# Kernel tuning notes

Hardware: AMD Instinct MI355X
Metric: run time of the kernel (lower is better)

## Reference

```python
import jax, jax.numpy as jnp
import numpy as np

B, S, DIN, D, H, DOUT, W = 4, 2048, 256, 512, 8, 128, 64
HD = D // H


def setup_inputs() -> dict:
    key = jax.random.key(0)
    ks = jax.random.split(key, 16)
    r = lambda k, shape, s=0.02: (jax.random.normal(k, shape, jnp.float32) * s)
    return dict(
        x=jax.random.normal(ks[0], (B, S, DIN), jnp.float32),
        pos=jax.random.normal(ks[1], (1, S, D), jnp.float32),  # torch.randn init
        win_w=r(ks[2], (DIN, D)), win_b=jnp.zeros((D,), jnp.float32),
        l_wqkv=r(ks[3], (3, D, D)), l_bqkv=jnp.zeros((3, D), jnp.float32),
        l_wo=r(ks[4], (D, D)), l_bo=jnp.zeros((D,), jnp.float32),
        g_wqkv=r(ks[5], (3, D, D)), g_bqkv=jnp.zeros((3, D), jnp.float32),
        g_wo=r(ks[6], (D, D)), g_bo=jnp.zeros((D,), jnp.float32),
        gate_w=r(ks[7], (2 * D, D)), gate_b=jnp.zeros((D,), jnp.float32),
        ffn_w1=r(ks[8], (D, 2 * D)), ffn_b1=jnp.zeros((2 * D,), jnp.float32),
        ffn_w2=r(ks[9], (2 * D, D)), ffn_b2=jnp.zeros((D,), jnp.float32),
        n1_g=jnp.ones((D,), jnp.float32), n1_b=jnp.zeros((D,), jnp.float32),
        n2_g=jnp.ones((D,), jnp.float32), n2_b=jnp.zeros((D,), jnp.float32),
        n3_g=jnp.ones((D,), jnp.float32), n3_b=jnp.zeros((D,), jnp.float32),
        out_w=r(ks[10], (D, DOUT)), out_b=jnp.zeros((DOUT,), jnp.float32),
    )


def _ln(x, g, b, eps=1e-5):
    m = x.mean(-1, keepdims=True)
    v = ((x - m) ** 2).mean(-1, keepdims=True)
    return (x - m) * jax.lax.rsqrt(v + eps) * g + b


def _mha(x, wqkv, bqkv, wo, bo, mask):
    b, s, d = x.shape
    q = (x @ wqkv[0] + bqkv[0]).reshape(b, s, H, HD)
    k = (x @ wqkv[1] + bqkv[1]).reshape(b, s, H, HD)
    v = (x @ wqkv[2] + bqkv[2]).reshape(b, s, H, HD)
    scores = jnp.einsum('bqhd,bkhd->bhqk', q, k) / np.sqrt(HD).astype(np.float32)
    if mask is not None:
        scores = scores + mask  # additive -inf band mask
    attn = jax.nn.softmax(scores, axis=-1)
    o = jnp.einsum('bhqk,bkhd->bqhd', attn, v).reshape(b, s, d)
    return o @ wo + bo


def reference(x, pos, win_w, win_b,
              l_wqkv, l_bqkv, l_wo, l_bo,
              g_wqkv, g_bqkv, g_wo, g_bo,
              gate_w, gate_b, ffn_w1, ffn_b1, ffn_w2, ffn_b2,
              n1_g, n1_b, n2_g, n2_b, n3_g, n3_b, out_w, out_b):
    s = x.shape[1]
    # band mask: row i allows cols [i - W//2, i + W//2] (matches create_local_mask)
    idx = jnp.arange(s)
    band = jnp.abs(idx[:, None] - idx[None, :]) <= (W // 2)
    mask = jnp.where(band, 0.0, -jnp.inf).astype(jnp.float32)

    h = x @ win_w + win_b + pos
    local_out = _mha(h, l_wqkv, l_bqkv, l_wo, l_bo, mask)
    global_out = _mha(h, g_wqkv, g_bqkv, g_wo, g_bo, None)

    combined = jnp.concatenate([local_out, global_out], axis=-1)
    gate = jnp.tanh(jax.nn.relu(combined @ gate_w + gate_b))
    fused = gate * local_out + (1.0 - gate) * global_out

    h = _ln(h + fused, n1_g, n1_b)
    ffn = jax.nn.relu(h @ ffn_w1 + ffn_b1) @ ffn_w2 + ffn_b2
    h = _ln(h + ffn, n2_g, n2_b)
    h = _ln(h, n3_g, n3_b)
    pooled = h.mean(axis=1)  # AdaptiveAvgPool1d(1) over seq
    return pooled @ out_w + out_b
```

## Files before the change

### kernel.cpp

```cpp
#include <hip/hip_runtime.h>
#include <math.h>
#include <stdint.h>

#define S_LEN 2048
#define DMODEL 512
#define NHEAD 8
#define BATCH 4
#define M_ROWS (BATCH * S_LEN)
#define UAC 4194304

typedef __attribute__((ext_vector_type(8))) short frag8;
typedef __attribute__((ext_vector_type(4))) float f32x4;

__device__ inline unsigned short f2bf(float f) {
    unsigned int u = __float_as_uint(f);
    return (unsigned short)((u + 0x7FFFu + ((u >> 16) & 1u)) >> 16);
}
__device__ inline float bf2f(unsigned short h) {
    return __uint_as_float(((unsigned int)h) << 16);
}

#if __has_builtin(__builtin_amdgcn_exp2f)
#define EXP2(x) __builtin_amdgcn_exp2f(x)
#else
#define EXP2(x) __expf(0.6931471805599453f * (x))
#endif

#if __has_builtin(__builtin_amdgcn_global_load_lds)
__device__ __forceinline__ void glds16(const void* g, void* l, int lane) {
    __builtin_amdgcn_global_load_lds(
        (__attribute__((address_space(1))) void*)(uintptr_t)g,
        (__attribute__((address_space(3))) void*)(uintptr_t)l, 16, 0, 0);
    (void)lane;
}
#else
__device__ __forceinline__ void glds16(const void* g, void* l, int lane) {
    ((uint4*)l)[lane] = ((const uint4*)g)[0];
}
#endif

struct WSeg { const float* src; unsigned short* dst; int K; int N; int start; };
struct WTab { WSeg s[12]; };

__global__ __launch_bounds__(256) void wcast_all(WTab tab)
{
    __shared__ float t[32][33];
    const int bid = blockIdx.x;
    int si = 0;
#pragma unroll
    for (int i = 1; i < 12; ++i) if (bid >= tab.s[i].start) si = i;
    const WSeg sg = tab.s[si];
    const int tile = bid - sg.start;
    const int nk = sg.K >> 5;
    const int k0 = (tile % nk) * 32, n0 = (tile / nk) * 32;
    {
        int kk = threadIdx.x >> 3, nq = (threadIdx.x & 7) * 4;
        float4 v = *(const float4*)&sg.src[(size_t)(k0 + kk) * sg.N + n0 + nq];
        t[kk][nq + 0] = v.x; t[kk][nq + 1] = v.y; t[kk][nq + 2] = v.z; t[kk][nq + 3] = v.w;
    }
    __syncthreads();
    {
        int n = threadIdx.x >> 3, kq = (threadIdx.x & 7) * 4;
        ushort4 o;
        o.x = f2bf(t[kq + 0][n]); o.y = f2bf(t[kq + 1][n]);
        o.z = f2bf(t[kq + 2][n]); o.w = f2bf(t[kq + 3][n]);
        *(ushort4*)&sg.dst[(size_t)(n0 + n) * sg.K + k0 + kq] = o;
    }
}

__global__ __launch_bounds__(256) void castx_kernel(
    const float* __restrict__ x, unsigned short* __restrict__ xb)
{
    const size_t i = ((size_t)blockIdx.x * 256 + threadIdx.x) * 8;
    float4 a = *(const float4*)&x[i], b = *(const float4*)&x[i + 4];
    unsigned short us[8];
    us[0] = f2bf(a.x); us[1] = f2bf(a.y); us[2] = f2bf(a.z); us[3] = f2bf(a.w);
    us[4] = f2bf(b.x); us[5] = f2bf(b.y); us[6] = f2bf(b.z); us[7] = f2bf(b.w);
    *(uint4*)&xb[i] = *(uint4*)us;
}

__global__ __launch_bounds__(256) void vtrans2_kernel(
    const unsigned short* __restrict__ Vl, const unsigned short* __restrict__ Vg,
    unsigned short* __restrict__ VTl, unsigned short* __restrict__ VTg)
{
    __shared__ unsigned short T[64][72];
    const unsigned short* V = blockIdx.z ? Vg : Vl;
    unsigned short* Vt = blockIdx.z ? VTg : VTl;
    const int st = blockIdx.x, bh = blockIdx.y;
    const int b = bh >> 3, h = bh & 7;
    const int tid = threadIdx.x;
    {
        const int s = tid >> 2, d0 = (tid & 3) * 16;
        const unsigned short* src = V + ((size_t)(b * S_LEN + st * 64 + s) * DMODEL + h * 64 + d0);
        *(uint4*)&T[s][d0] = *(const uint4*)src;
        *(uint4*)&T[s][d0 + 8] = *(const uint4*)(src + 8);
    }
    __syncthreads();
    {
        const int d = tid >> 2, s0 = (tid & 3) * 16;
        unsigned short buf[16];
#pragma unroll
        for (int j = 0; j < 16; ++j) buf[j] = T[s0 + j][d];
        unsigned short* dst = Vt + ((size_t)(bh * 64 + d) * S_LEN + st * 64 + s0);
        *(uint4*)&dst[0] = *(const uint4*)&buf[0];
        *(uint4*)&dst[8] = *(const uint4*)&buf[8];
    }
}

template <int MODE, int BN>
__global__ __launch_bounds__(256) void gemm_mfma(
    const unsigned short* __restrict__ A, const unsigned short* __restrict__ A2,
    const unsigned short* __restrict__ Wt, const float* __restrict__ bias,
    const float* __restrict__ bias2, const float* __restrict__ pos,
    unsigned short* __restrict__ C, unsigned short* __restrict__ C2,
    int M, int N, int K)
{
    constexpr int UN = BN / 32;
    __shared__ unsigned short As[128 * 64];
    __shared__ unsigned short Bs[BN * 64];
    const int tid = threadIdx.x;
    const int wave = tid >> 6, lane = tid & 63;
    const int lr = lane & 15, quad = lane >> 4;
    const int bm = blockIdx.x * 128, bn = blockIdx.y * BN;
    const int rm = (wave >> 1) * 64, rn = (wave & 1) * (BN / 2);
    const int Khalf = K >> 1;
    const int KA = (MODE == 3) ? Khalf : K;

    const unsigned short* SA = A;
    const unsigned short* SW = Wt;
    const float* SBIAS = bias;
    unsigned short* SC = C;
    if constexpr (MODE == 6) {
        if (blockIdx.z) { SA = A2; SW = Wt + 512 * 512; SBIAS = bias2; SC = C2; }
    }

    const int lrow = lane >> 3;
    const int gch = ((lane & 7) - lrow) & 7;
    const size_t laneA = (size_t)(bm + wave * 32 + lrow) * KA + gch * 8;
    const size_t laneB = (size_t)(bn + wave * (BN / 4) + lrow) * K + gch * 8;
    unsigned short* ldsA = As + wave * 2048;
    unsigned short* ldsB = Bs + wave * (BN * 16);

    f32x4 acc[4][UN];
#pragma unroll
    for (int t = 0; t < 4; ++t)
#pragma unroll
        for (int u = 0; u < UN; ++u) acc[t][u] = (f32x4){0.f, 0.f, 0.f, 0.f};

    const int sw0 = ((quad + lr) & 7) * 8;
    const int sw1 = ((quad + lr + 4) & 7) * 8;

    for (int k0 = 0; k0 < K; k0 += 64) {
        __syncthreads();
        const unsigned short* Ab; int kadj;
        if constexpr (MODE == 3) { Ab = (k0 < Khalf) ? A : A2; kadj = k0 & (Khalf - 1); }
        else { Ab = SA; kadj = k0; }
        const unsigned short* pa = Ab + laneA + kadj;
        glds16(pa,           ldsA,        lane);
        glds16(pa + 8 * KA,  ldsA + 512,  lane);
        glds16(pa + 16 * KA, ldsA + 1024, lane);
        glds16(pa + 24 * KA, ldsA + 1536, lane);
        const unsigned short* pb = SW + laneB + k0;
#pragma unroll
        for (int i = 0; i < UN; ++i)
            glds16(pb + i * 8 * K, ldsB + i * 512, lane);
        __syncthreads();

#pragma unroll
        for (int kc = 0; kc < 2; ++kc) {
            const int sw = kc ? sw1 : sw0;
            frag8 af[4], bf[UN];
#pragma unroll
            for (int t = 0; t < 4; ++t)
                af[t] = *(const frag8*)&As[(rm + t * 16 + lr) * 64 + sw];
#pragma unroll
            for (int u = 0; u < UN; ++u)
                bf[u] = *(const frag8*)&Bs[(rn + u * 16 + lr) * 64 + sw];
#pragma unroll
            for (int t = 0; t < 4; ++t)
#pragma unroll
                for (int u = 0; u < UN; ++u)
                    acc[t][u] = __builtin_amdgcn_mfma_f32_16x16x32_bf16(
                        af[t], bf[u], acc[t][u], 0, 0, 0);
        }
    }

#pragma unroll
    for (int t = 0; t < 4; ++t) {
#pragma unroll
        for (int i = 0; i < 4; ++i) {
            const int m = bm + rm + t * 16 + quad * 4 + i;
#pragma unroll
            for (int u = 0; u < UN; ++u) {
                const int n = bn + rn + u * 16 + lr;
                if constexpr (MODE == 5) {
                    const int mat = n >> 9;
                    const int nn = n & 511;
                    const float* bp = (mat < 3) ? (bias + (mat << 9))
                                                : (bias2 + ((mat - 3) << 9));
                    float v = acc[t][u][i] + bp[nn];
                    if (mat == 0 || mat == 3) v *= 0.18033688011112042f;
                    C[(size_t)mat * UAC + (size_t)m * DMODEL + nn] = f2bf(v);
                } else {
                    float v = acc[t][u][i] + SBIAS[n];
                    if constexpr (MODE == 1) v += pos[(size_t)(m & (S_LEN - 1)) * N + n];
                    if constexpr (MODE == 2) v = fmaxf(v, 0.0f);
                    if constexpr (MODE == 3) {
                        float g = tanhf(fmaxf(v, 0.0f));
                        float lo = bf2f(A[(size_t)m * Khalf + n]);
                        float go = bf2f(A2[(size_t)m * Khalf + n]);
                        v = g * lo + (1.0f - g) * go;
                    }
                    SC[(size_t)m * N + n] = f2bf(v);
                }
            }
        }
    }
}

__global__ __launch_bounds__(256) void attn_mfma(
    const unsigned short* __restrict__ Ql, const unsigned short* __restrict__ Kl,
    const unsigned short* __restrict__ VTl, unsigned short* __restrict__ Ol,
    const unsigned short* __restrict__ Qg, const unsigned short* __restrict__ Kg,
    const unsigned short* __restrict__ VTg, unsigned short* __restrict__ Og)
{
    __shared__ unsigned short Ks[64 * 64];
    __shared__ unsigned short Vts[64 * 64];
    __shared__ unsigned short Ps[128 * 64];
    const int qt = blockIdx.x, h = blockIdx.y;
    const int glob = blockIdx.z >> 2, b = blockIdx.z & 3;
    const int masked = !glob;
    const unsigned short* Q  = glob ? Qg  : Ql;
    const unsigned short* Kv = glob ? Kg  : Kl;
    const unsigned short* Vt = glob ? VTg : VTl;
    unsigned short* O        = glob ? Og  : Ol;
    const int tid = threadIdx.x;
    const int wave = tid >> 6, lane = tid & 63;
    const int lr = lane & 15, quad = lane >> 4;

    {
        const int q = tid >> 1, cb = (tid & 1) * 4;
        const unsigned short* src = Q + ((size_t)(b * S_LEN + qt * 128 + q) * DMODEL + h * 64 + cb * 8);
#pragma unroll
        for (int i = 0; i < 4; ++i)
            *(uint4*)&Ps[q * 64 + (((cb + i + q) & 7) * 8)] = *(const uint4*)(src + i * 8);
    }
    const int sw0 = ((quad + lr) & 7) * 8;
    const int sw1 = ((quad + lr + 4) & 7) * 8;
    const int ws32 = wave * 32;
    frag8 qf[2][2];
#pragma unroll
    for (int s = 0; s < 2; ++s) {
        qf[s][0] = *(const frag8*)&Ps[(ws32 + s * 16 + lr) * 64 + sw0];
        qf[s][1] = *(const frag8*)&Ps[(ws32 + s * 16 + lr) * 64 + sw1];
    }

    f32x4 oacc[2][4];
#pragma unroll
    for (int s = 0; s < 2; ++s)
#pragma unroll
        for (int t = 0; t < 4; ++t) oacc[s][t] = (f32x4){0.f, 0.f, 0.f, 0.f};
    float l_r[2] = {0.f, 0.f};

    int kt0 = 0, kt1 = 31;
    if (masked) {
        kt0 = qt * 128 >= 32 ? (qt * 128 - 32) >> 6 : 0;
        int hi = (qt * 128 + 127 + 32) >> 6;
        kt1 = hi < 31 ? hi : 31;
    }

    const int lrow = lane >> 3;
    const int gch = ((lane & 7) - lrow) & 7;
    const unsigned short* kp = Kv + ((size_t)(b * S_LEN + kt0 * 64 + wave * 16 + lrow) * DMODEL + h * 64 + gch * 8);
    const unsigned short* vp = Vt + ((size_t)((b * 8 + h) * 64 + wave * 16 + lrow) * S_LEN + kt0 * 64 + gch * 8);
    unsigned short* lk = Ks + wave * 1024;
    unsigned short* lv = Vts + wave * 1024;

    for (int kt = kt0; kt <= kt1; ++kt) {
        __syncthreads();
        glds16(kp, lk, lane);
        glds16(kp + 8 * DMODEL, lk + 512, lane);
        glds16(vp, lv, lane);
        glds16(vp + 8 * S_LEN, lv + 512, lane);
        kp += 64 * DMODEL; vp += 64;
        __syncthreads();

        f32x4 sacc[2][4];
#pragma unroll
        for (int s = 0; s < 2; ++s)
#pragma unroll
            for (int t = 0; t < 4; ++t) sacc[s][t] = (f32x4){0.f, 0.f, 0.f, 0.f};
#pragma unroll
        for (int kc = 0; kc < 2; ++kc) {
            const int sw = kc ? sw1 : sw0;
#pragma unroll
            for (int t = 0; t < 4; ++t) {
                frag8 kf = *(const frag8*)&Ks[(t * 16 + lr) * 64 + sw];
                sacc[0][t] = __builtin_amdgcn_mfma_f32_16x16x32_bf16(kf, qf[0][kc], sacc[0][t], 0, 0, 0);
                sacc[1][t] = __builtin_amdgcn_mfma_f32_16x16x32_bf16(kf, qf[1][kc], sacc[1][t], 0, 0, 0);
            }
        }

#pragma unroll
        for (int s = 0; s < 2; ++s) {
            const int prow = (ws32 + s * 16 + lr) * 64;
#pragma unroll
            for (int t = 0; t < 4; ++t) {
                float p0 = EXP2(sacc[s][t][0]);
                float p1 = EXP2(sacc[s][t][1]);
                float p2 = EXP2(sacc[s][t][2]);
                float p3 = EXP2(sacc[s][t][3]);
                if (masked) {
                    const int qa = qt * 128 + ws32 + s * 16 + lr;
                    const int ca = kt * 64 + t * 16 + quad * 4;
                    int d0 = qa - ca;
                    if (d0 > 32 || d0 < -32) p0 = 0.f;
                    int d1 = qa - (ca + 1);
                    if (d1 > 32 || d1 < -32) p1 = 0.f;
                    int d2 = qa - (ca + 2);
                    if (d2 > 32 || d2 < -32) p2 = 0.f;
                    int d3 = qa - (ca + 3);
                    if (d3 > 32 || d3 < -32) p3 = 0.f;
                }
                const unsigned u0 = __float_as_uint(p0) & 0xFFFF0000u;
                const unsigned u1 = __float_as_uint(p1) & 0xFFFF0000u;
                const unsigned u2 = __float_as_uint(p2) & 0xFFFF0000u;
                const unsigned u3 = __float_as_uint(p3) & 0xFFFF0000u;
                l_r[s] += (__uint_as_float(u0) + __uint_as_float(u1)) +
                          (__uint_as_float(u2) + __uint_as_float(u3));
                uint2 pw;
                pw.x = __builtin_amdgcn_perm(u1, u0, 0x07060302);
                pw.y = __builtin_amdgcn_perm(u3, u2, 0x07060302);
                const int slot = ((2 * t + (quad >> 1) + lr) & 7) * 8 + (quad & 1) * 4;
                *(uint2*)&Ps[prow + slot] = pw;
            }
        }

#pragma unroll
        for (int cc = 0; cc < 2; ++cc) {
            const int sw = cc ? sw1 : sw0;
            frag8 pa0 = *(const frag8*)&Ps[(ws32 + lr) * 64 + sw];
            frag8 pa1 = *(const frag8*)&Ps[(ws32 + 16 + lr) * 64 + sw];
#pragma unroll
            for (int t = 0; t < 4; ++t) {
                frag8 vf = *(const frag8*)&Vts[(t * 16 + lr) * 64 + sw];
                oacc[0][t] = __builtin_amdgcn_mfma_f32_16x16x32_bf16(pa0, vf, oacc[0][t], 0, 0, 0);
                oacc[1][t] = __builtin_amdgcn_mfma_f32_16x16x32_bf16(pa1, vf, oacc[1][t], 0, 0, 0);
            }
        }
    }

#pragma unroll
    for (int s = 0; s < 2; ++s) {
        float l = l_r[s];
        l += __shfl_xor(l, 16);
        l += __shfl_xor(l, 32);
#pragma unroll
        for (int i = 0; i < 4; ++i) {
            const float inv = 1.0f / __shfl(l, quad * 4 + i);
            const int q = qt * 128 + ws32 + s * 16 + quad * 4 + i;
#pragma unroll
            for (int t = 0; t < 4; ++t)
                O[(size_t)(b * S_LEN + q) * DMODEL + h * 64 + t * 16 + lr] =
                    f2bf(oacc[s][t][i] * inv);
        }
    }
}

__device__ inline float wave_sum64(float v) {
#pragma unroll
    for (int off = 1; off < 64; off <<= 1) v += __shfl_xor(v, off);
    return v;
}

__global__ __launch_bounds__(256) void ln_res_kernel(
    const unsigned short* __restrict__ A, const unsigned short* __restrict__ Bb,
    const float* __restrict__ g, const float* __restrict__ be,
    unsigned short* __restrict__ out)
{
    const size_t row = blockIdx.x * 4 + (threadIdx.x >> 6);
    const int lane = threadIdx.x & 63;
    float x[8]; float s = 0.f;
#pragma unroll
    for (int k = 0; k < 8; ++k) {
        size_t idx = row * DMODEL + k * 64 + lane;
        x[k] = bf2f(A[idx]) + bf2f(Bb[idx]);
        s += x[k];
    }
    s = wave_sum64(s);
    float mean = s * (1.0f / DMODEL);
    float v = 0.f;
#pragma unroll
    for (int k = 0; k < 8; ++k) { float d = x[k] - mean; v += d * d; }
    v = wave_sum64(v) * (1.0f / DMODEL);
    float r = rsqrtf(v + 1e-5f);
#pragma unroll
    for (int k = 0; k < 8; ++k)
        out[row * DMODEL + k * 64 + lane] =
            f2bf((x[k] - mean) * r * g[k * 64 + lane] + be[k * 64 + lane]);
}

__global__ __launch_bounds__(256) void ln_double_kernel(
    const unsigned short* __restrict__ A, const unsigned short* __restrict__ Bb,
    const float* __restrict__ g2, const float* __restrict__ b2,
    const float* __restrict__ g3, const float* __restrict__ b3,
    unsigned short* __restrict__ out)
{
    const size_t row = blockIdx.x * 4 + (threadIdx.x >> 6);
    const int lane = threadIdx.x & 63;
    float x[8]; float s = 0.f;
#pragma unroll
    for (int k = 0; k < 8; ++k) {
        size_t idx = row * DMODEL + k * 64 + lane;
        x[k] = bf2f(A[idx]) + bf2f(Bb[idx]);
        s += x[k];
    }
    s = wave_sum64(s);
    float mean = s * (1.0f / DMODEL);
    float v = 0.f;
#pragma unroll
    for (int k = 0; k < 8; ++k) { float d = x[k] - mean; v += d * d; }
    v = wave_sum64(v) * (1.0f / DMODEL);
    float r = rsqrtf(v + 1e-5f);
    float t[8]; float s2 = 0.f;
#pragma unroll
    for (int k = 0; k < 8; ++k) {
        t[k] = (x[k] - mean) * r * g2[k * 64 + lane] + b2[k * 64 + lane];
        s2 += t[k];
    }
    s2 = wave_sum64(s2);
    float mean2 = s2 * (1.0f / DMODEL);
    float v2 = 0.f;
#pragma unroll
    for (int k = 0; k < 8; ++k) { float d = t[k] - mean2; v2 += d * d; }
    v2 = wave_sum64(v2) * (1.0f / DMODEL);
    float r2 = rsqrtf(v2 + 1e-5f);
#pragma unroll
    for (int k = 0; k < 8; ++k)
        out[row * DMODEL + k * 64 + lane] =
            f2bf((t[k] - mean2) * r2 * g3[k * 64 + lane] + b3[k * 64 + lane]);
}

__global__ __launch_bounds__(256) void pool_kernel(
    const unsigned short* __restrict__ h2, float* __restrict__ pooled)
{
    const int b = blockIdx.x >> 4;
    const int chunk = blockIdx.x & 15;
    const int tid = threadIdx.x;
    float s0 = 0.f, s1 = 0.f;
    size_t base = (size_t)(b * S_LEN + chunk * 128) * DMODEL;
    for (int r = 0; r < 128; ++r) {
        s0 += bf2f(h2[base + (size_t)r * DMODEL + tid]);
        s1 += bf2f(h2[base + (size_t)r * DMODEL + 256 + tid]);
    }
    atomicAdd(&pooled[b * DMODEL + tid], s0);
    atomicAdd(&pooled[b * DMODEL + 256 + tid], s1);
}

__global__ __launch_bounds__(128) void out_kernel(
    const float* __restrict__ pooled, const float* __restrict__ w,
    const float* __restrict__ bias, float* __restrict__ out)
{
    const int b = blockIdx.x;
    const int o = threadIdx.x;
    float acc = 0.f;
    for (int d = 0; d < DMODEL; ++d)
        acc += pooled[b * DMODEL + d] * w[d * 128 + o];
    out[b * 128 + o] = acc * (1.0f / S_LEN) + bias[o];
}

extern "C" void kernel_launch(void* const* d_in, const int* in_sizes, int n_in,
                              void* d_out, int out_size, void* d_ws, size_t ws_size,
                              hipStream_t stream)
{
    const float* x      = (const float*)d_in[0];
    const float* pos    = (const float*)d_in[1];
    const float* win_w  = (const float*)d_in[2];
    const float* win_b  = (const float*)d_in[3];
    const float* l_wqkv = (const float*)d_in[4];
    const float* l_bqkv = (const float*)d_in[5];
    const float* l_wo   = (const float*)d_in[6];
    const float* l_bo   = (const float*)d_in[7];
    const float* g_wqkv = (const float*)d_in[8];
    const float* g_bqkv = (const float*)d_in[9];
    const float* g_wo   = (const float*)d_in[10];
    const float* g_bo   = (const float*)d_in[11];
    const float* gate_w = (const float*)d_in[12];
    const float* gate_b = (const float*)d_in[13];
    const float* ffn_w1 = (const float*)d_in[14];
    const float* ffn_b1 = (const float*)d_in[15];
    const float* ffn_w2 = (const float*)d_in[16];
    const float* ffn_b2 = (const float*)d_in[17];
    const float* n1_g   = (const float*)d_in[18];
    const float* n1_b   = (const float*)d_in[19];
    const float* n2_g   = (const float*)d_in[20];
    const float* n2_b   = (const float*)d_in[21];
    const float* n3_g   = (const float*)d_in[22];
    const float* n3_b   = (const float*)d_in[23];
    const float* out_w  = (const float*)d_in[24];
    const float* out_b  = (const float*)d_in[25];
    float* out = (float*)d_out;

    unsigned short* ws16 = (unsigned short*)d_ws;
    const size_t UA = (size_t)UAC;
    unsigned short* H    = ws16 + 0 * UA;
    unsigned short* QKV  = ws16 + 1 * UA;
    unsigned short* Ql   = ws16 + 1 * UA;
    unsigned short* Kl   = ws16 + 2 * UA;
    unsigned short* Vl   = ws16 + 3 * UA;
    unsigned short* Qg   = ws16 + 4 * UA;
    unsigned short* Kg   = ws16 + 5 * UA;
    unsigned short* Vg   = ws16 + 6 * UA;
    unsigned short* VTl  = ws16 + 7 * UA;
    unsigned short* AOl    = Vl;
    unsigned short* LO     = Kl;
    unsigned short* GO     = Qg;
    unsigned short* FUSED  = Kg;
    unsigned short* H1     = Vg;
    unsigned short* FFNMID = Vl;
    unsigned short* FFNOUT = Ql;
    unsigned short* H2     = Kl;
    float* POOLED = (float*)(void*)H;

    unsigned short* wt = ws16 + 8 * UA;
    unsigned short* win_t  = wt;
    unsigned short* lqkv_t = win_t  + 131072;
    unsigned short* gqkv_t = lqkv_t + 786432;
    unsigned short* lwo_t  = gqkv_t + 786432;
    unsigned short* gwo_t  = lwo_t  + 262144;
    unsigned short* gate_t = gwo_t  + 262144;
    unsigned short* ffn1_t = gate_t + 524288;
    unsigned short* ffn2_t = ffn1_t + 524288;
    unsigned short* xb     = ffn2_t + 524288;
    unsigned short* VTg    = xb + 2097152;
    unsigned short* AOg    = VTg + UA;

    WTab tab;
    tab.s[0]  = {win_w,             win_t,             256,  512,    0};
    tab.s[1]  = {l_wqkv + 0*262144, lqkv_t + 0*262144, 512,  512,  128};
    tab.s[2]  = {l_wqkv + 1*262144, lqkv_t + 1*262144, 512,  512,  384};
    tab.s[3]  = {l_wqkv + 2*262144, lqkv_t + 2*262144, 512,  512,  640};
    tab.s[4]  = {g_wqkv + 0*262144, gqkv_t + 0*262144, 512,  512,  896};
    tab.s[5]  = {g_wqkv + 1*262144, gqkv_t + 1*262144, 512,  512, 1152};
    tab.s[6]  = {g_wqkv + 2*262144, gqkv_t + 2*262144, 512,  512, 1408};
    tab.s[7]  = {l_wo,              lwo_t,             512,  512, 1664};
    tab.s[8]  = {g_wo,              gwo_t,             512,  512, 1920};
    tab.s[9]  = {gate_w,            gate_t,            1024, 512, 2176};
    tab.s[10] = {ffn_w1,            ffn1_t,            512, 1024, 2688};
    tab.s[11] = {ffn_w2,            ffn2_t,            1024, 512, 3200};

    dim3 blk(256);
    castx_kernel<<<dim3(1024), blk, 0, stream>>>(x, xb);
    wcast_all<<<dim3(3712), blk, 0, stream>>>(tab);

    dim3 gD(M_ROWS / 128, 512 / 64);
    dim3 gW(M_ROWS / 128, 512 / 64, 2);
    dim3 gQ(M_ROWS / 128, 3072 / 128);
    dim3 gF(M_ROWS / 128, 1024 / 128);
    dim3 gAT(S_LEN / 128, NHEAD, 2*BATCH);
    dim3 gV(S_LEN / 64, BATCH * NHEAD, 2);

    gemm_mfma<1, 64><<<gD, blk, 0, stream>>>(xb, nullptr, win_t, win_b, nullptr, pos, H, nullptr, M_ROWS, 512, 256);

    gemm_mfma<5, 128><<<gQ, blk, 0, stream>>>(H, nullptr, lqkv_t, l_bqkv, g_bqkv, nullptr, QKV, nullptr, M_ROWS, 3072, 512);

    vtrans2_kernel<<<gV, blk, 0, stream>>>(Vl, Vg, VTl, VTg);

    attn_mfma<<<gAT, blk, 0, stream>>>(Ql, Kl, VTl, AOl, Qg, Kg, VTg, AOg);

    gemm_mfma<6, 64><<<gW, blk, 0, stream>>>(AOl, AOg, lwo_t, l_bo, g_bo, nullptr, LO, GO, M_ROWS, 512, 512);

    gemm_mfma<3, 64><<<gD, blk, 0, stream>>>(LO, GO, gate_t, gate_b, nullptr, nullptr, FUSED, nullptr, M_ROWS, 512, 1024);

    ln_res_kernel<<<M_ROWS / 4, blk, 0, stream>>>(H, FUSED, n1_g, n1_b, H1);

    gemm_mfma<2, 128><<<gF, blk, 0, stream>>>(H1, nullptr, ffn1_t, ffn_b1, nullptr, nullptr, FFNMID, nullptr, M_ROWS, 1024, 512);
    gemm_mfma<0, 64><<<gD, blk, 0, stream>>>(FFNMID, nullptr, ffn2_t, ffn_b2, nullptr, nullptr, FFNOUT, nullptr, M_ROWS, 512, 1024);

    ln_double_kernel<<<M_ROWS / 4, blk, 0, stream>>>(H1, FFNOUT, n2_g, n2_b, n3_g, n3_b, H2);

    hipMemsetAsync(POOLED, 0, BATCH * DMODEL * sizeof(float), stream);
    pool_kernel<<<dim3(BATCH * 16), blk, 0, stream>>>(H2, POOLED);
    out_kernel<<<dim3(BATCH), dim3(128), 0, stream>>>(POOLED, out_w, out_b, out);
}
```

Baseline: 368.6 us.

## Split attention into local and global kernels with double-buffered KV

Replaces the combined local/global attention kernel with two specialized kernels. The local kernel uses 64-row query tiles so each block visits only three KV tiles, which cuts wasted band work and removes the masked/unmasked branching. The global kernel drops the mask code and double-buffers K/V tiles in LDS so the next tile's loads overlap the current tile's compute. The trade-offs are an extra kernel launch, the two attention types no longer sharing one grid, and doubled LDS use in the global kernel, which may lower occupancy.

```diff
diff --git a/kernel.cpp b/kernel.cpp
--- a/kernel.cpp
+++ b/kernel.cpp
@@ -218,56 +218,38 @@
     }
 }
 
-__global__ __launch_bounds__(256) void attn_mfma(
-    const unsigned short* __restrict__ Ql, const unsigned short* __restrict__ Kl,
-    const unsigned short* __restrict__ VTl, unsigned short* __restrict__ Ol,
-    const unsigned short* __restrict__ Qg, const unsigned short* __restrict__ Kg,
-    const unsigned short* __restrict__ VTg, unsigned short* __restrict__ Og)
+__global__ __launch_bounds__(256) void attn_local(
+    const unsigned short* __restrict__ Q, const unsigned short* __restrict__ Kv,
+    const unsigned short* __restrict__ Vt, unsigned short* __restrict__ O)
 {
     __shared__ unsigned short Ks[64 * 64];
     __shared__ unsigned short Vts[64 * 64];
-    __shared__ unsigned short Ps[128 * 64];
-    const int qt = blockIdx.x, h = blockIdx.y;
-    const int glob = blockIdx.z >> 2, b = blockIdx.z & 3;
-    const int masked = !glob;
-    const unsigned short* Q  = glob ? Qg  : Ql;
-    const unsigned short* Kv = glob ? Kg  : Kl;
-    const unsigned short* Vt = glob ? VTg : VTl;
-    unsigned short* O        = glob ? Og  : Ol;
+    __shared__ unsigned short Ps[64 * 64];
+    const int qt = blockIdx.x, h = blockIdx.y, b = blockIdx.z;
     const int tid = threadIdx.x;
     const int wave = tid >> 6, lane = tid & 63;
     const int lr = lane & 15, quad = lane >> 4;
 
     {
-        const int q = tid >> 1, cb = (tid & 1) * 4;
-        const unsigned short* src = Q + ((size_t)(b * S_LEN + qt * 128 + q) * DMODEL + h * 64 + cb * 8);
-#pragma unroll
-        for (int i = 0; i < 4; ++i)
-            *(uint4*)&Ps[q * 64 + (((cb + i + q) & 7) * 8)] = *(const uint4*)(src + i * 8);
+        const int q = tid >> 2, c8 = (tid & 3) * 2;
+        const unsigned short* src = Q + ((size_t)(b * S_LEN + qt * 64 + q) * DMODEL + h * 64 + c8 * 8);
+        *(uint4*)&Ps[q * 64 + (((c8 + q) & 7) * 8)] = *(const uint4*)src;
+        *(uint4*)&Ps[q * 64 + (((c8 + 1 + q) & 7) * 8)] = *(const uint4*)(src + 8);
     }
     const int sw0 = ((quad + lr) & 7) * 8;
     const int sw1 = ((quad + lr + 4) & 7) * 8;
-    const int ws32 = wave * 32;
-    frag8 qf[2][2];
-#pragma unroll
-    for (int s = 0; s < 2; ++s) {
-        qf[s][0] = *(const frag8*)&Ps[(ws32 + s * 16 + lr) * 64 + sw0];
-        qf[s][1] = *(const frag8*)&Ps[(ws32 + s * 16 + lr) * 64 + sw1];
-    }
-
-    f32x4 oacc[2][4];
-#pragma unroll
-    for (int s = 0; s < 2; ++s)
-#pragma unroll
-        for (int t = 0; t < 4; ++t) oacc[s][t] = (f32x4){0.f, 0.f, 0.f, 0.f};
-    float l_r[2] = {0.f, 0.f};
-
-    int kt0 = 0, kt1 = 31;
-    if (masked) {
-        kt0 = qt * 128 >= 32 ? (qt * 128 - 32) >> 6 : 0;
-        int hi = (qt * 128 + 127 + 32) >> 6;
-        kt1 = hi < 31 ? hi : 31;
-    }
+    const int prow = (wave * 16 + lr) * 64;
+    frag8 qf[2];
+    qf[0] = *(const frag8*)&Ps[prow + sw0];
+    qf[1] = *(const frag8*)&Ps[prow + sw1];
+
+    f32x4 oacc[4];
+#pragma unroll
+    for (int t = 0; t < 4; ++t) oacc[t] = (f32x4){0.f, 0.f, 0.f, 0.f};
+    float l_r = 0.f;
+
+    const int kt0 = qt > 0 ? qt - 1 : 0;
+    const int kt1 = qt < 31 ? qt + 1 : 31;
 
     const int lrow = lane >> 3;
     const int gch = ((lane & 7) - lrow) & 7;
@@ -285,17 +267,142 @@
         kp += 64 * DMODEL; vp += 64;
         __syncthreads();
 
-        f32x4 sacc[2][4];
-#pragma unroll
-        for (int s = 0; s < 2; ++s)
-#pragma unroll
-            for (int t = 0; t < 4; ++t) sacc[s][t] = (f32x4){0.f, 0.f, 0.f, 0.f};
+        f32x4 sacc[4];
+#pragma unroll
+        for (int t = 0; t < 4; ++t) sacc[t] = (f32x4){0.f, 0.f, 0.f, 0.f};
 #pragma unroll
         for (int kc = 0; kc < 2; ++kc) {
             const int sw = kc ? sw1 : sw0;
 #pragma unroll
             for (int t = 0; t < 4; ++t) {
                 frag8 kf = *(const frag8*)&Ks[(t * 16 + lr) * 64 + sw];
+                sacc[t] = __builtin_amdgcn_mfma_f32_16x16x32_bf16(kf, qf[kc], sacc[t], 0, 0, 0);
+            }
+        }
+
+#pragma unroll
+        for (int t = 0; t < 4; ++t) {
+            float p0 = EXP2(sacc[t][0]);
+            float p1 = EXP2(sacc[t][1]);
+            float p2 = EXP2(sacc[t][2]);
+            float p3 = EXP2(sacc[t][3]);
+            const int qa = qt * 64 + wave * 16 + lr;
+            const int ca = kt * 64 + t * 16 + quad * 4;
+            int d0 = qa - ca;
+            if (d0 > 32 || d0 < -32) p0 = 0.f;
+            int d1 = qa - (ca + 1);
+            if (d1 > 32 || d1 < -32) p1 = 0.f;
+            int d2 = qa - (ca + 2);
+            if (d2 > 32 || d2 < -32) p2 = 0.f;
+            int d3 = qa - (ca + 3);
+            if (d3 > 32 || d3 < -32) p3 = 0.f;
+            const unsigned u0 = __float_as_uint(p0) & 0xFFFF0000u;
+            const unsigned u1 = __float_as_uint(p1) & 0xFFFF0000u;
+            const unsigned u2 = __float_as_uint(p2) & 0xFFFF0000u;
+            const unsigned u3 = __float_as_uint(p3) & 0xFFFF0000u;
+            l_r += (__uint_as_float(u0) + __uint_as_float(u1)) +
+                   (__uint_as_float(u2) + __uint_as_float(u3));
+            uint2 pw;
+            pw.x = __builtin_amdgcn_perm(u1, u0, 0x07060302);
+            pw.y = __builtin_amdgcn_perm(u3, u2, 0x07060302);
+            const int slot = ((2 * t + (quad >> 1) + lr) & 7) * 8 + (quad & 1) * 4;
+            *(uint2*)&Ps[prow + slot] = pw;
+        }
+
+#pragma unroll
+        for (int cc = 0; cc < 2; ++cc) {
+            const int sw = cc ? sw1 : sw0;
+            frag8 pa = *(const frag8*)&Ps[prow + sw];
+#pragma unroll
+            for (int t = 0; t < 4; ++t) {
+                frag8 vf = *(const frag8*)&Vts[(t * 16 + lr) * 64 + sw];
+                oacc[t] = __builtin_amdgcn_mfma_f32_16x16x32_bf16(pa, vf, oacc[t], 0, 0, 0);
+            }
+        }
+    }
+
+    l_r += __shfl_xor(l_r, 16);
+    l_r += __shfl_xor(l_r, 32);
+#pragma unroll
+    for (int i = 0; i < 4; ++i) {
+        const float inv = 1.0f / __shfl(l_r, quad * 4 + i);
+        const int q = qt * 64 + wave * 16 + quad * 4 + i;
+#pragma unroll
+        for (int t = 0; t < 4; ++t)
+            O[(size_t)(b * S_LEN + q) * DMODEL + h * 64 + t * 16 + lr] = f2bf(oacc[t][i] * inv);
+    }
+}
+
+#define ISSUE_KV_G(KT, BUF) do {                                                \
+    const unsigned short* _kp = kbase + (size_t)(KT) * (64 * DMODEL);           \
+    const unsigned short* _vp = vbase + (size_t)(KT) * 64;                      \
+    unsigned short* _lk = Ks + (BUF) * 4096 + wave * 1024;                      \
+    unsigned short* _lv = Vts + (BUF) * 4096 + wave * 1024;                     \
+    glds16(_kp, _lk, lane); glds16(_kp + 8 * DMODEL, _lk + 512, lane);          \
+    glds16(_vp, _lv, lane); glds16(_vp + 8 * S_LEN, _lv + 512, lane);           \
+} while (0)
+
+__global__ __launch_bounds__(256) void attn_global(
+    const unsigned short* __restrict__ Q, const unsigned short* __restrict__ Kv,
+    const unsigned short* __restrict__ Vt, unsigned short* __restrict__ O)
+{
+    __shared__ unsigned short Ks[2 * 64 * 64];
+    __shared__ unsigned short Vts[2 * 64 * 64];
+    __shared__ unsigned short Ps[128 * 64];
+    const int qt = blockIdx.x, h = blockIdx.y, b = blockIdx.z;
+    const int tid = threadIdx.x;
+    const int wave = tid >> 6, lane = tid & 63;
+    const int lr = lane & 15, quad = lane >> 4;
+
+    {
+        const int q = tid >> 1, cb = (tid & 1) * 4;
+        const unsigned short* src = Q + ((size_t)(b * S_LEN + qt * 128 + q) * DMODEL + h * 64 + cb * 8);
+#pragma unroll
+        for (int i = 0; i < 4; ++i)
+            *(uint4*)&Ps[q * 64 + (((cb + i + q) & 7) * 8)] = *(const uint4*)(src + i * 8);
+    }
+    const int sw0 = ((quad + lr) & 7) * 8;
+    const int sw1 = ((quad + lr + 4) & 7) * 8;
+    const int ws32 = wave * 32;
+    frag8 qf[2][2];
+#pragma unroll
+    for (int s = 0; s < 2; ++s) {
+        qf[s][0] = *(const frag8*)&Ps[(ws32 + s * 16 + lr) * 64 + sw0];
+        qf[s][1] = *(const frag8*)&Ps[(ws32 + s * 16 + lr) * 64 + sw1];
+    }
+
+    f32x4 oacc[2][4];
+#pragma unroll
+    for (int s = 0; s < 2; ++s)
+#pragma unroll
+        for (int t = 0; t < 4; ++t) oacc[s][t] = (f32x4){0.f, 0.f, 0.f, 0.f};
+    float l_r[2] = {0.f, 0.f};
+
+    const int lrow = lane >> 3;
+    const int gch = ((lane & 7) - lrow) & 7;
+    const unsigned short* kbase = Kv + ((size_t)(b * S_LEN + wave * 16 + lrow) * DMODEL + h * 64 + gch * 8);
+    const unsigned short* vbase = Vt + ((size_t)((b * 8 + h) * 64 + wave * 16 + lrow) * S_LEN + gch * 8);
+
+    ISSUE_KV_G(0, 0);
+
+    for (int it = 0; it < 32; ++it) {
+        const int buf = it & 1;
+        __syncthreads();
+        if (it + 1 < 32) ISSUE_KV_G(it + 1, buf ^ 1);
+        const unsigned short* kb = Ks + buf * 4096;
+        const unsigned short* vb = Vts + buf * 4096;
+
+        f32x4 sacc[2][4];
+#pragma unroll
+        for (int s = 0; s < 2; ++s)
+#pragma unroll
+            for (int t = 0; t < 4; ++t) sacc[s][t] = (f32x4){0.f, 0.f, 0.f, 0.f};
+#pragma unroll
+        for (int kc = 0; kc < 2; ++kc) {
+            const int sw = kc ? sw1 : sw0;
+#pragma unroll
+            for (int t = 0; t < 4; ++t) {
+                frag8 kf = *(const frag8*)&kb[(t * 16 + lr) * 64 + sw];
                 sacc[0][t] = __builtin_amdgcn_mfma_f32_16x16x32_bf16(kf, qf[0][kc], sacc[0][t], 0, 0, 0);
                 sacc[1][t] = __builtin_amdgcn_mfma_f32_16x16x32_bf16(kf, qf[1][kc], sacc[1][t], 0, 0, 0);
             }
@@ -306,26 +413,10 @@
             const int prow = (ws32 + s * 16 + lr) * 64;
 #pragma unroll
             for (int t = 0; t < 4; ++t) {
-                float p0 = EXP2(sacc[s][t][0]);
-                float p1 = EXP2(sacc[s][t][1]);
-                float p2 = EXP2(sacc[s][t][2]);
-                float p3 = EXP2(sacc[s][t][3]);
-                if (masked) {
-                    const int qa = qt * 128 + ws32 + s * 16 + lr;
-                    const int ca = kt * 64 + t * 16 + quad * 4;
-                    int d0 = qa - ca;
-                    if (d0 > 32 || d0 < -32) p0 = 0.f;
-                    int d1 = qa - (ca + 1);
-                    if (d1 > 32 || d1 < -32) p1 = 0.f;
-                    int d2 = qa - (ca + 2);
-                    if (d2 > 32 || d2 < -32) p2 = 0.f;
-                    int d3 = qa - (ca + 3);
-                    if (d3 > 32 || d3 < -32) p3 = 0.f;
-                }
-                const unsigned u0 = __float_as_uint(p0) & 0xFFFF0000u;
-                const unsigned u1 = __float_as_uint(p1) & 0xFFFF0000u;
-                const unsigned u2 = __float_as_uint(p2) & 0xFFFF0000u;
-                const unsigned u3 = __float_as_uint(p3) & 0xFFFF0000u;
+                const unsigned u0 = __float_as_uint(EXP2(sacc[s][t][0])) & 0xFFFF0000u;
+                const unsigned u1 = __float_as_uint(EXP2(sacc[s][t][1])) & 0xFFFF0000u;
+                const unsigned u2 = __float_as_uint(EXP2(sacc[s][t][2])) & 0xFFFF0000u;
+                const unsigned u3 = __float_as_uint(EXP2(sacc[s][t][3])) & 0xFFFF0000u;
                 l_r[s] += (__uint_as_float(u0) + __uint_as_float(u1)) +
                           (__uint_as_float(u2) + __uint_as_float(u3));
                 uint2 pw;
@@ -343,7 +434,7 @@
             frag8 pa1 = *(const frag8*)&Ps[(ws32 + 16 + lr) * 64 + sw];
 #pragma unroll
             for (int t = 0; t < 4; ++t) {
-                frag8 vf = *(const frag8*)&Vts[(t * 16 + lr) * 64 + sw];
+                frag8 vf = *(const frag8*)&vb[(t * 16 + lr) * 64 + sw];
                 oacc[0][t] = __builtin_amdgcn_mfma_f32_16x16x32_bf16(pa0, vf, oacc[0][t], 0, 0, 0);
                 oacc[1][t] = __builtin_amdgcn_mfma_f32_16x16x32_bf16(pa1, vf, oacc[1][t], 0, 0, 0);
             }
@@ -557,7 +648,8 @@
     dim3 gW(M_ROWS / 128, 512 / 64, 2);
     dim3 gQ(M_ROWS / 128, 3072 / 128);
     dim3 gF(M_ROWS / 128, 1024 / 128);
-    dim3 gAT(S_LEN / 128, NHEAD, 2*BATCH);
+    dim3 gAL(S_LEN / 64, NHEAD, BATCH);
+    dim3 gAG(S_LEN / 128, NHEAD, BATCH);
     dim3 gV(S_LEN / 64, BATCH * NHEAD, 2);
 
     gemm_mfma<1, 64><<<gD, blk, 0, stream>>>(xb, nullptr, win_t, win_b, nullptr, pos, H, nullptr, M_ROWS, 512, 256);
@@ -566,7 +658,8 @@
 
     vtrans2_kernel<<<gV, blk, 0, stream>>>(Vl, Vg, VTl, VTg);
 
-    attn_mfma<<<gAT, blk, 0, stream>>>(Ql, Kl, VTl, AOl, Qg, Kg, VTg, AOg);
+    attn_local<<<gAL, blk, 0, stream>>>(Ql, Kl, VTl, AOl);
+    attn_global<<<gAG, blk, 0, stream>>>(Qg, Kg, VTg, AOg);
 
     gemm_mfma<6, 64><<<gW, blk, 0, stream>>>(AOl, AOg, lwo_t, l_bo, g_bo, nullptr, LO, GO, M_ROWS, 512, 512);
 
```

After: 378.5 us. +2.7%, slower.
